# Optimization experiments

Hardware: AMD Instinct MI355X
Metric: run time of the kernel (lower is better)

Reference implementation:

```python
import jax, jax.numpy as jnp
import numpy as np

E = 8   # num_experts
K = 2   # experts per token


def setup_inputs() -> dict:
    key = jax.random.key(0)
    k1, k2, k3, k4 = jax.random.split(key, 4)
    B, S, H, F = 8, 2048, 1024, 2048
    x = jax.random.normal(k1, (B, S, H), jnp.float32)
    Wg = jax.random.normal(k2, (H, E), jnp.float32) * 0.02
    W1 = jax.random.normal(k3, (E, H, F), jnp.float32) * 0.02
    W2 = jax.random.normal(k4, (E, F, H), jnp.float32) * 0.02
    return {"x": x, "Wg": Wg, "W1": W1, "W2": W2}


def reference(x, Wg, W1, W2):
    orig_shape = x.shape
    xt = x.reshape(-1, orig_shape[-1])          # [T, H]
    T = xt.shape[0]

    # router (no jitter noise: training=False path)
    router_logits = xt @ Wg                     # [T, E]
    routing_weights = jax.nn.softmax(router_logits, axis=-1)
    expert_weights, expert_indices = jax.lax.top_k(routing_weights, K)  # [T, K]

    # router z-loss (float32, as in source)
    log_z = jax.nn.logsumexp(router_logits.astype(jnp.float32), axis=-1)
    z_loss = jnp.sum(log_z * log_z) / T

    # load-balancing loss, faithful to source: num_experts taken from
    # router_probs.shape[-1] == K, and one_hot(expert_indices, K)
    # (out-of-range indices -> zero rows under jax.nn.one_hot semantics)
    oh_k = jax.nn.one_hot(expert_indices, K, dtype=jnp.float32)  # [T, K, K]
    expert_mask = jnp.max(oh_k, axis=-2)                          # [T, K]
    tokens_per_expert = jnp.mean(expert_mask, axis=0)             # [K]
    router_prob_per_expert = jnp.mean(expert_weights.astype(jnp.float32), axis=0)  # [K]
    aux_loss = jnp.mean(tokens_per_expert * router_prob_per_expert) * (K ** 2)

    # combine weight per (token, expert): sum of top-k weights routed to e
    cw = jnp.einsum('tk,tke->te', expert_weights,
                    jax.nn.one_hot(expert_indices, E, dtype=expert_weights.dtype))  # [T, E]

    # per-expert MLP, weighted combine (loop over small fixed E)
    out = jnp.zeros_like(xt)
    for e in range(E):
        h = jax.nn.gelu(xt @ W1[e], approximate=False)  # [T, F]
        out = out + cw[:, e:e + 1] * (h @ W2[e])        # [T, H]

    return out.reshape(orig_shape), z_loss, aux_loss
```

## Files before the change

### kernel.cpp

```cpp
#include <hip/hip_runtime.h>
#include <math.h>

#define T_TOKENS 16384
#define H_DIM 1024
#define F_DIM 2048
#define E_NUM 8
#define TPR 72
#define TOT_T (2 * TPR)
#define MAX_PAIRS (TOT_T * 256)

typedef __attribute__((ext_vector_type(8))) short bf16x8;
typedef __attribute__((ext_vector_type(4))) float f32x4;
typedef __attribute__((ext_vector_type(4))) unsigned short us4;

struct TopK { int e0, e1; float w0, w1; };

__device__ __forceinline__ unsigned short f2bf(float f) {
  unsigned int u = __float_as_uint(f);
  u = (u + 0x7fffu + ((u >> 16) & 1u)) >> 16;
  return (unsigned short)u;
}

__device__ __forceinline__ float bf2f(unsigned short u) {
  return __uint_as_float(((unsigned int)u) << 16);
}

__device__ __forceinline__ void gload_lds16(const void* g, void* l) {
  __builtin_amdgcn_global_load_lds(
      (const __attribute__((address_space(1))) void*)g,
      (__attribute__((address_space(3))) void*)l, 16, 0, 0);
}

__device__ __forceinline__ void transpose_body(
    const float* __restrict__ in, unsigned short* __restrict__ out,
    int R, int C, int bx, int by, int e, float* tile ) {
  int r0 = by * 64, c0 = bx * 64;
  int tid = threadIdx.x;
  const float* src = in + ((size_t)e * R + r0) * C + c0;
#pragma unroll
  for (int p = 0; p < 4; p++) {
    int id = p * 256 + tid;
    int row = id >> 4, c4 = (id & 15) * 4;
    float4 v = *(const float4*)&src[(size_t)row * C + c4];
    tile[row * 65 + c4 + 0] = v.x; tile[row * 65 + c4 + 1] = v.y;
    tile[row * 65 + c4 + 2] = v.z; tile[row * 65 + c4 + 3] = v.w;
  }
  __syncthreads();
  unsigned short* dst = out + ((size_t)e * C + c0) * R + r0;
#pragma unroll
  for (int p = 0; p < 4; p++) {
    int id = p * 256 + tid;
    int c = id >> 4, r4 = (id & 15) * 4;
    us4 pk;
#pragma unroll
    for (int j = 0; j < 4; j++) pk[j] = f2bf(tile[(r4 + j) * 65 + c]);
    *(us4*)&dst[(size_t)c * R + r4] = pk;
  }
}

__global__ __launch_bounds__(256) void prep_kernel(
    const float* __restrict__ x, const float* __restrict__ Wg,
    const float* __restrict__ W1, const float* __restrict__ W2,
    unsigned short* __restrict__ xb, unsigned short* __restrict__ w1t,
    unsigned short* __restrict__ w2t, TopK* __restrict__ topk,
    int* __restrict__ counts, float* __restrict__ scal) {
  __shared__ __align__(16) char shraw[E_NUM * H_DIM * 4 + 256];
  int bid = blockIdx.x;
  int tid = threadIdx.x;
  if (bid >= 1024) {
    float* tile = (float*)shraw;
    if (bid < 5120) {
      int lb = bid - 1024;
      transpose_body(W1, w1t, H_DIM, F_DIM, lb & 31, (lb >> 5) & 15, lb >> 9, tile);
    } else {
      int lb = bid - 5120;
      transpose_body(W2, w2t, F_DIM, H_DIM, lb & 15, (lb >> 4) & 31, lb >> 9, tile);
    }
    return;
  }
  float (*wg)[H_DIM] = (float(*)[H_DIM])shraw;
  int* cnt = (int*)(shraw + E_NUM * H_DIM * 4);
  float (*sred)[5] = (float(*)[5])(shraw + E_NUM * H_DIM * 4 + 64);
  if (tid < 16) cnt[tid] = 0;
  for (int i = tid; i < E_NUM * H_DIM; i += 256) wg[i & 7][i >> 3] = Wg[i];
  __syncthreads();
  int lane = tid & 63, wid = tid >> 6;
  float zacc = 0.f, c0 = 0.f, c1 = 0.f, s0 = 0.f, s1 = 0.f;
  int wgid = bid * 4 + wid;
#pragma unroll
  for (int it = 0; it < 4; ++it) {
    int t = wgid + it * 4096;
    const float4* xr = (const float4*)(x + (size_t)t * H_DIM);
    us4* xbr = (us4*)(xb + (size_t)t * H_DIM);
    float l[E_NUM];
#pragma unroll
    for (int e = 0; e < E_NUM; e++) l[e] = 0.f;
#pragma unroll
    for (int i = 0; i < 4; i++) {
      int j = i * 64 + lane;
      float4 v = xr[j];
      us4 pk;
      pk[0] = f2bf(v.x); pk[1] = f2bf(v.y); pk[2] = f2bf(v.z); pk[3] = f2bf(v.w);
      xbr[j] = pk;
      int h = j * 4;
#pragma unroll
      for (int e = 0; e < E_NUM; e++) {
        const f32x4 wv = *(const f32x4*)&wg[e][h];
        l[e] = fmaf(v.x, wv[0], l[e]);
        l[e] = fmaf(v.y, wv[1], l[e]);
        l[e] = fmaf(v.z, wv[2], l[e]);
        l[e] = fmaf(v.w, wv[3], l[e]);
      }
    }
#pragma unroll
    for (int off = 32; off > 0; off >>= 1) {
#pragma unroll
      for (int e = 0; e < E_NUM; e++) l[e] += __shfl_xor(l[e], off, 64);
    }
    if (lane == 0) {
      float mx = l[0];
#pragma unroll
      for (int e = 1; e < E_NUM; e++) mx = fmaxf(mx, l[e]);
      float p[E_NUM]; float se = 0.f;
#pragma unroll
      for (int e = 0; e < E_NUM; e++) { p[e] = expf(l[e] - mx); se += p[e]; }
      float logz = logf(se) + mx;
      int e0 = 0; float b0 = p[0];
#pragma unroll
      for (int e = 1; e < E_NUM; e++) if (p[e] > b0) { b0 = p[e]; e0 = e; }
      int e1 = -1; float b1 = -1.f;
#pragma unroll
      for (int e = 0; e < E_NUM; e++) if (e != e0 && p[e] > b1) { b1 = p[e]; e1 = e; }
      float w0 = b0 / se, w1 = b1 / se;
      TopK tk; tk.e0 = e0; tk.e1 = e1; tk.w0 = w0; tk.w1 = w1;
      topk[t] = tk;
      atomicAdd(&cnt[e0], 1);
      atomicAdd(&cnt[8 + e1], 1);
      zacc += logz * logz;
      c0 += (e0 == 0 || e1 == 0) ? 1.f : 0.f;
      c1 += (e0 == 1 || e1 == 1) ? 1.f : 0.f;
      s0 += w0; s1 += w1;
    }
  }
  if (lane == 0) {
    sred[wid][0] = zacc; sred[wid][1] = c0; sred[wid][2] = c1;
    sred[wid][3] = s0;   sred[wid][4] = s1;
  }
  __syncthreads();
  if (tid == 0) {
    float a[5] = {0.f, 0.f, 0.f, 0.f, 0.f};
    for (int w2 = 0; w2 < 4; w2++)
      for (int k = 0; k < 5; k++) a[k] += sred[w2][k];
    for (int k = 0; k < 5; k++) atomicAdd(&scal[k], a[k]);
  }
  if (tid < 16 && cnt[tid]) atomicAdd(&counts[tid], cnt[tid]);
}

__global__ __launch_bounds__(256) void scan_kernel(
    const int* __restrict__ counts, int* __restrict__ po,
    int* __restrict__ tile_expert) {
  __shared__ int nt[16], start[16];
  int tid = threadIdx.x;
  if (tid < 16) {
    int r = tid >> 3, e = tid & 7;
    int s = 0;
    for (int j = 0; j < e; j++) s += (counts[(r << 3) + j] + 255) >> 8;
    nt[tid] = (counts[tid] + 255) >> 8;
    start[tid] = s;
    po[tid] = r * TPR * 256 + (s << 8);
  }
  __syncthreads();
  for (int ti = tid; ti < TOT_T; ti += 256) {
    int r = ti / TPR, local = ti % TPR;
    int ex = -1;
#pragma unroll
    for (int e = 0; e < E_NUM; e++) {
      int k = (r << 3) + e;
      if (local >= start[k] && local < start[k] + nt[k]) ex = e;
    }
    tile_expert[ti] = ex;
  }
}

__global__ __launch_bounds__(256) void assign_kernel(
    const TopK* __restrict__ topk, const int* __restrict__ po,
    int* __restrict__ cursors, int* __restrict__ pair_token,
    float* __restrict__ pair_w, int* __restrict__ inv0, int* __restrict__ inv1) {
  __shared__ int lcnt[16], lbase[16];
  int tid = threadIdx.x;
  if (tid < 16) lcnt[tid] = 0;
  __syncthreads();
  int t = blockIdx.x * 256 + tid;
  TopK tk = topk[t];
  int li0 = atomicAdd(&lcnt[tk.e0], 1);
  int li1 = atomicAdd(&lcnt[8 + tk.e1], 1);
  __syncthreads();
  if (tid < 16) lbase[tid] = lcnt[tid] ? atomicAdd(&cursors[tid], lcnt[tid]) : 0;
  __syncthreads();
  int p0 = po[tk.e0] + lbase[tk.e0] + li0;
  pair_token[p0] = t; pair_w[p0] = tk.w0; inv0[t] = p0;
  int p1 = po[8 + tk.e1] + lbase[8 + tk.e1] + li1;
  pair_token[p1] = t; pair_w[p1] = tk.w1; inv1[t] = p1;
}

template <int MODE, int K, int N, int NTILES>
__global__ __launch_bounds__(512) void moe_gemm8(
    const unsigned short* __restrict__ A, const unsigned short* __restrict__ Bt,
    const int* __restrict__ pair_token, const float* __restrict__ pair_w,
    const int* __restrict__ tile_expert, int tile_base,
    unsigned short* __restrict__ outbf) {
  constexpr int NBN = N / 256;
  constexpr int NTk = K / 64;
  constexpr int MTC = NTILES / 8;
  constexpr int OSTRIDE = (MODE == 0) ? N : K;
  int l = blockIdx.x;
  int xcd = l & 7, idx = l >> 3;
  int mt = tile_base + xcd * MTC + idx / NBN;
  int nb = idx % NBN;
  int e = tile_expert[mt];
  if (e < 0) return;
  int m0 = mt << 8, n0 = nb << 8;

  extern __shared__ __align__(16) char smem_raw[];
  unsigned short* lds = (unsigned short*)smem_raw;

  int tid = threadIdx.x, lane = tid & 63, wid = tid >> 6;
  int wm = wid >> 2, wn = wid & 3;
  int lo = lane & 15, hi = lane >> 4;
  int l7 = lane & 7;

  int aRB = (wm * 64 + lo) * 64;
  int bRB = (wn * 32 + lo) * 64;
  int kd0 = (hi ^ l7) * 8;
  int kd1 = ((4 + hi) ^ l7) * 8;

  int kcs = ((tid & 7) ^ ((tid >> 3) & 7)) * 8;
  int rr = tid >> 3;
  const unsigned short *aSrc[2][2], *bSrc[2][2];
#pragma unroll
  for (int qa = 0; qa < 2; qa++)
#pragma unroll
    for (int j = 0; j < 2; j++) {
      int row = j * 128 + qa * 64 + rr;
      size_t off;
      if (MODE == 0) {
        int tk = pair_token[m0 + row]; if (tk < 0) tk = 0;
        off = (size_t)tk * K;
      } else {
        off = (size_t)(m0 + row) * K;
      }
      aSrc[qa][j] = A + off + kcs;
    }
#pragma unroll
  for (int qb = 0; qb < 2; qb++)
#pragma unroll
    for (int j = 0; j < 2; j++) {
      int rp = j * 64 + rr;
      int col = (rp >> 5) * 64 + qb * 32 + (rp & 31);
      bSrc[qb][j] = Bt + ((size_t)e * N + n0 + col) * K + kcs;
    }

#define ST0(src, qa, s, sb) do { \
    gload_lds16(src[qa][0] + (size_t)(s) * 64, lds + (sb) + wid * 512); \
    gload_lds16(src[qa][1] + (size_t)(s) * 64, lds + (sb) + 4096 + wid * 512); } while (0)
#define ST_P(ptr, base, g) do { if (g) { \
    gload_lds16(ptr[0], lds + (base) + wid * 512); \
    gload_lds16(ptr[1], lds + (base) + 4096 + wid * 512); \
    ptr[0] += 64; ptr[1] += 64; } } while (0)
#define RD_A(dst, qa, rb) do { _Pragma("unroll") \
    for (int mf = 0; mf < 4; mf++) { \
      dst[mf * 2 + 0] = *(const bf16x8*)&lds[(rb) + (qa) * 8192 + aRB + mf * 1024 + kd0]; \
      dst[mf * 2 + 1] = *(const bf16x8*)&lds[(rb) + (qa) * 8192 + aRB + mf * 1024 + kd1]; } } while (0)
#define RD_B(dst, qb, rb) do { _Pragma("unroll") \
    for (int nf = 0; nf < 2; nf++) { \
      dst[nf * 2 + 0] = *(const bf16x8*)&lds[(rb) + 16384 + (qb) * 8192 + bRB + nf * 1024 + kd0]; \
      dst[nf * 2 + 1] = *(const bf16x8*)&lds[(rb) + 16384 + (qb) * 8192 + bRB + nf * 1024 + kd1]; } } while (0)
#define MMQ(aq, bq, QA, QB) do { __builtin_amdgcn_s_setprio(1); _Pragma("unroll") \
    for (int mf = 0; mf < 4; mf++) _Pragma("unroll") \
    for (int nf = 0; nf < 2; nf++) { \
      acc[(QA) * 4 + mf][(QB) * 2 + nf] = __builtin_amdgcn_mfma_f32_16x16x32_bf16( \
          bq[nf * 2 + 0], aq[mf * 2 + 0], acc[(QA) * 4 + mf][(QB) * 2 + nf], 0, 0, 0); \
      acc[(QA) * 4 + mf][(QB) * 2 + nf] = __builtin_amdgcn_mfma_f32_16x16x32_bf16( \
          bq[nf * 2 + 1], aq[mf * 2 + 1], acc[(QA) * 4 + mf][(QB) * 2 + nf], 0, 0, 0); } \
    __builtin_amdgcn_s_setprio(0); } while (0)
#define PH_BAR() do { asm volatile("s_barrier" ::: "memory"); \
    __builtin_amdgcn_sched_barrier(0); } while (0)
#define VMC(n) do { asm volatile("s_waitcnt vmcnt(" #n ")" ::: "memory"); \
    __builtin_amdgcn_sched_barrier(0); } while (0)

  f32x4 acc[8][4];
#pragma unroll
  for (int i = 0; i < 8; i++)
#pragma unroll
    for (int j = 0; j < 4; j++) acc[i][j] = (f32x4){0.f, 0.f, 0.f, 0.f};

  bf16x8 afr[8], bfr0[4], bfr1[4];

  ST0(aSrc, 0, 0, 0); ST0(bSrc, 0, 0, 16384); ST0(bSrc, 1, 0, 24576); ST0(aSrc, 1, 0, 8192);
  ST0(aSrc, 0, 1, 32768); ST0(bSrc, 0, 1, 32768 + 16384);
  VMC(4); PH_BAR();

  const unsigned short* pB1[2] = {bSrc[1][0] + 64, bSrc[1][1] + 64};
  const unsigned short* pA1[2] = {aSrc[1][0] + 64, aSrc[1][1] + 64};
  const unsigned short* pA0[2] = {aSrc[0][0] + 128, aSrc[0][1] + 128};
  const unsigned short* pB0[2] = {bSrc[0][0] + 128, bSrc[0][1] + 128};

#pragma unroll 2
  for (int t = 0; t < NTk; ++t) {
    int bo = (t & 1) << 15, bn = bo ^ 32768;
    bool g1 = (t + 1 < NTk), g2 = (t + 2 < NTk);
    RD_A(afr, 0, bo);
    RD_B(bfr0, 0, bo);
    ST_P(pB1, bn + 24576, g1);
    VMC(8); PH_BAR();
    MMQ(afr, bfr0, 0, 0);
    RD_B(bfr1, 1, bo);
    ST_P(pA1, bn + 8192, g1);
    PH_BAR();
    MMQ(afr, bfr1, 0, 1);
    RD_A(afr, 1, bo);
    ST_P(pA0, bo, g2);
    VMC(8); PH_BAR();
    MMQ(afr, bfr1, 1, 1);
    ST_P(pB0, bo + 16384, g2);
    PH_BAR();
    MMQ(afr, bfr0, 1, 0);
  }
  asm volatile("s_waitcnt vmcnt(0)" ::: "memory");
  __builtin_amdgcn_sched_barrier(0);
#undef ST0
#undef ST_P
#undef RD_A
#undef RD_B
#undef MMQ
#undef PH_BAR
#undef VMC

#pragma unroll
  for (int mh = 0; mh < 2; mh++)
#pragma unroll
    for (int mf = 0; mf < 4; mf++) {
      size_t p = m0 + wm * 128 + mh * 64 + mf * 16 + lo;
      float w = (MODE == 0) ? 0.f : pair_w[p];
#pragma unroll
      for (int nf = 0; nf < 4; nf++) {
        int f = n0 + wn * 64 + nf * 16 + hi * 4;
        us4 pk;
#pragma unroll
        for (int r = 0; r < 4; r++) {
          float v = acc[mh * 4 + mf][nf][r];
          if (MODE == 0) {
            float u = fmaf(0.044715f * v * v, v, v);
            float s = 1.f / (1.f + __expf(-1.5957691216057308f * u));
            pk[r] = f2bf(v * s);
          } else {
            pk[r] = f2bf(w * v);
          }
        }
        *(us4*)&outbf[p * (size_t)OSTRIDE + f] = pk;
      }
    }
}

__global__ __launch_bounds__(256) void combine_kernel(
    const unsigned short* __restrict__ hout, const int* __restrict__ inv0,
    const int* __restrict__ inv1, float* __restrict__ outp,
    const float* __restrict__ scal) {
  int idx = blockIdx.x * 256 + threadIdx.x;
  int t = idx >> 7;
  int c = (idx & 127) * 8;
  int p0 = inv0[t], p1 = inv1[t];
  bf16x8 va = *(const bf16x8*)&hout[(size_t)p0 * F_DIM + c];
  bf16x8 vb = *(const bf16x8*)&hout[(size_t)p1 * F_DIM + c];
  float* orow = outp + (size_t)t * H_DIM + c;
  float4 o0, o1;
  o0.x = bf2f((unsigned short)va[0]) + bf2f((unsigned short)vb[0]);
  o0.y = bf2f((unsigned short)va[1]) + bf2f((unsigned short)vb[1]);
  o0.z = bf2f((unsigned short)va[2]) + bf2f((unsigned short)vb[2]);
  o0.w = bf2f((unsigned short)va[3]) + bf2f((unsigned short)vb[3]);
  o1.x = bf2f((unsigned short)va[4]) + bf2f((unsigned short)vb[4]);
  o1.y = bf2f((unsigned short)va[5]) + bf2f((unsigned short)vb[5]);
  o1.z = bf2f((unsigned short)va[6]) + bf2f((unsigned short)vb[6]);
  o1.w = bf2f((unsigned short)va[7]) + bf2f((unsigned short)vb[7]);
  *(float4*)&orow[0] = o0;
  *(float4*)&orow[4] = o1;
  if (idx == 0) {
    float invT = 1.f / (float)T_TOKENS;
    float* outTail = outp + (size_t)T_TOKENS * H_DIM;
    outTail[0] = scal[0] * invT;
    float tpe0 = scal[1] * invT, tpe1 = scal[2] * invT;
    float rp0 = scal[3] * invT, rp1 = scal[4] * invT;
    outTail[1] = (tpe0 * rp0 + tpe1 * rp1) * 0.5f * 4.f;
  }
}

extern "C" void kernel_launch(void* const* d_in, const int* in_sizes, int n_in,
                              void* d_out, int out_size, void* d_ws, size_t ws_size,
                              hipStream_t stream) {
  const float* x  = (const float*)d_in[0];
  const float* Wg = (const float*)d_in[1];
  const float* W1 = (const float*)d_in[2];
  const float* W2 = (const float*)d_in[3];
  float* outp = (float*)d_out;

  char* w = (char*)d_ws;
  auto alloc = [&](size_t b) { char* p = w; w += (b + 511) & ~(size_t)511; return p; };
  char*  meta        = alloc(256);
  float* scal        = (float*)(meta + 0);
  int*   counts      = (int*)(meta + 64);
  int*   cursors     = (int*)(meta + 128);
  int*   po          = (int*)alloc(64);
  int*   tile_expert = (int*)alloc(TOT_T * 4);
  TopK*  topk        = (TopK*)alloc((size_t)T_TOKENS * sizeof(TopK));
  int*   pair_token  = (int*)alloc((size_t)MAX_PAIRS * 4);
  float* pair_w      = (float*)alloc((size_t)MAX_PAIRS * 4);
  int*   inv0        = (int*)alloc((size_t)T_TOKENS * 4);
  int*   inv1        = (int*)alloc((size_t)T_TOKENS * 4);
  unsigned short* xb   = (unsigned short*)alloc((size_t)T_TOKENS * H_DIM * 2 + 512);
  unsigned short* w1t  = (unsigned short*)alloc((size_t)E_NUM * F_DIM * H_DIM * 2 + 512);
  unsigned short* hmid = (unsigned short*)alloc((size_t)MAX_PAIRS * F_DIM * 2 + 512);
  unsigned short* w2t = (unsigned short*)d_out;

  hipFuncSetAttribute((const void*)&moe_gemm8<0, H_DIM, F_DIM, TOT_T>,
                      hipFuncAttributeMaxDynamicSharedMemorySize, 131072);
  hipFuncSetAttribute((const void*)&moe_gemm8<1, F_DIM, H_DIM, TOT_T>,
                      hipFuncAttributeMaxDynamicSharedMemorySize, 131072);

  hipMemsetAsync(meta, 0, 256, stream);
  hipMemsetAsync(pair_token, 0xFF, (size_t)MAX_PAIRS * 4, stream);

  dim3 b256(256), b512(512);
  prep_kernel<<<dim3(9216), b256, 0, stream>>>(x, Wg, W1, W2, xb, w1t, w2t,
                                               topk, counts, scal);
  scan_kernel<<<1, b256, 0, stream>>>(counts, po, tile_expert);
  assign_kernel<<<T_TOKENS / 256, b256, 0, stream>>>(topk, po, cursors, pair_token, pair_w,
                                                     inv0, inv1);
  moe_gemm8<0, H_DIM, F_DIM, TOT_T><<<dim3((F_DIM / 256) * TOT_T), b512, 131072, stream>>>(
      xb, w1t, pair_token, pair_w, tile_expert, 0, hmid);
  moe_gemm8<1, F_DIM, H_DIM, TOT_T><<<dim3((H_DIM / 256) * TOT_T), b512, 131072, stream>>>(
      hmid, w2t, pair_token, pair_w, tile_expert, 0, hmid);
  combine_kernel<<<dim3(T_TOKENS * 128 / 256), b256, 0, stream>>>(hmid, inv0, inv1, outp, scal);
}
```

Before: 472.1 us.

## Convert MoE GEMMs to persistent kernels with per-XCD atomic job tickets

Both expert GEMM kernels now launch a fixed grid of 256 persistent blocks instead of one block per (tile, column-block). Each block repeatedly takes a job index from a per-XCD atomic counter and skips empty expert tiles. The goal is to remove launch and exit cost for the many blocks that hit unused padded tiles, and to balance load within each XCD. In exchange it adds atomics and extra barriers per job, and the inner k-loop is no longer unrolled by 2 and now bounds-checks each prefetch.

```diff
diff --git a/kernel.cpp b/kernel.cpp
--- a/kernel.cpp
+++ b/kernel.cpp
@@ -207,22 +207,18 @@
 __global__ __launch_bounds__(512) void moe_gemm8(
     const unsigned short* __restrict__ A, const unsigned short* __restrict__ Bt,
     const int* __restrict__ pair_token, const float* __restrict__ pair_w,
-    const int* __restrict__ tile_expert, int tile_base,
+    const int* __restrict__ tile_expert, int* __restrict__ tickets,
     unsigned short* __restrict__ outbf) {
   constexpr int NBN = N / 256;
   constexpr int NTk = K / 64;
   constexpr int MTC = NTILES / 8;
+  constexpr int JOBS = NBN * MTC;
   constexpr int OSTRIDE = (MODE == 0) ? N : K;
-  int l = blockIdx.x;
-  int xcd = l & 7, idx = l >> 3;
-  int mt = tile_base + xcd * MTC + idx / NBN;
-  int nb = idx % NBN;
-  int e = tile_expert[mt];
-  if (e < 0) return;
-  int m0 = mt << 8, n0 = nb << 8;
+  int xcd = blockIdx.x & 7;
 
   extern __shared__ __align__(16) char smem_raw[];
   unsigned short* lds = (unsigned short*)smem_raw;
+  volatile int* ticket_slot = (volatile int*)lds;
 
   int tid = threadIdx.x, lane = tid & 63, wid = tid >> 6;
   int wm = wid >> 2, wn = wid & 3;
@@ -233,40 +229,15 @@
   int bRB = (wn * 32 + lo) * 64;
   int kd0 = (hi ^ l7) * 8;
   int kd1 = ((4 + hi) ^ l7) * 8;
-
   int kcs = ((tid & 7) ^ ((tid >> 3) & 7)) * 8;
   int rr = tid >> 3;
-  const unsigned short *aSrc[2][2], *bSrc[2][2];
-#pragma unroll
-  for (int qa = 0; qa < 2; qa++)
-#pragma unroll
-    for (int j = 0; j < 2; j++) {
-      int row = j * 128 + qa * 64 + rr;
-      size_t off;
-      if (MODE == 0) {
-        int tk = pair_token[m0 + row]; if (tk < 0) tk = 0;
-        off = (size_t)tk * K;
-      } else {
-        off = (size_t)(m0 + row) * K;
-      }
-      aSrc[qa][j] = A + off + kcs;
-    }
-#pragma unroll
-  for (int qb = 0; qb < 2; qb++)
-#pragma unroll
-    for (int j = 0; j < 2; j++) {
-      int rp = j * 64 + rr;
-      int col = (rp >> 5) * 64 + qb * 32 + (rp & 31);
-      bSrc[qb][j] = Bt + ((size_t)e * N + n0 + col) * K + kcs;
-    }
-
-#define ST0(src, qa, s, sb) do { \
-    gload_lds16(src[qa][0] + (size_t)(s) * 64, lds + (sb) + wid * 512); \
-    gload_lds16(src[qa][1] + (size_t)(s) * 64, lds + (sb) + 4096 + wid * 512); } while (0)
-#define ST_P(ptr, base, g) do { if (g) { \
-    gload_lds16(ptr[0], lds + (base) + wid * 512); \
-    gload_lds16(ptr[1], lds + (base) + 4096 + wid * 512); \
-    ptr[0] += 64; ptr[1] += 64; } } while (0)
+
+#define ST_A(qa, s, sb) do { if ((s) < NTk) { \
+    gload_lds16(aSrc[qa][0] + (size_t)(s) * 64, lds + (sb) + (qa) * 8192 + wid * 512); \
+    gload_lds16(aSrc[qa][1] + (size_t)(s) * 64, lds + (sb) + (qa) * 8192 + 4096 + wid * 512); } } while (0)
+#define ST_B(qb, s, sb) do { if ((s) < NTk) { \
+    gload_lds16(bSrc[qb][0] + (size_t)(s) * 64, lds + (sb) + 16384 + (qb) * 8192 + wid * 512); \
+    gload_lds16(bSrc[qb][1] + (size_t)(s) * 64, lds + (sb) + 16384 + (qb) * 8192 + 4096 + wid * 512); } } while (0)
 #define RD_A(dst, qa, rb) do { _Pragma("unroll") \
     for (int mf = 0; mf < 4; mf++) { \
       dst[mf * 2 + 0] = *(const bf16x8*)&lds[(rb) + (qa) * 8192 + aRB + mf * 1024 + kd0]; \
@@ -288,78 +259,108 @@
 #define VMC(n) do { asm volatile("s_waitcnt vmcnt(" #n ")" ::: "memory"); \
     __builtin_amdgcn_sched_barrier(0); } while (0)
 
-  f32x4 acc[8][4];
-#pragma unroll
-  for (int i = 0; i < 8; i++)
-#pragma unroll
-    for (int j = 0; j < 4; j++) acc[i][j] = (f32x4){0.f, 0.f, 0.f, 0.f};
-
-  bf16x8 afr[8], bfr0[4], bfr1[4];
-
-  ST0(aSrc, 0, 0, 0); ST0(bSrc, 0, 0, 16384); ST0(bSrc, 1, 0, 24576); ST0(aSrc, 1, 0, 8192);
-  ST0(aSrc, 0, 1, 32768); ST0(bSrc, 0, 1, 32768 + 16384);
-  VMC(4); PH_BAR();
-
-  const unsigned short* pB1[2] = {bSrc[1][0] + 64, bSrc[1][1] + 64};
-  const unsigned short* pA1[2] = {aSrc[1][0] + 64, aSrc[1][1] + 64};
-  const unsigned short* pA0[2] = {aSrc[0][0] + 128, aSrc[0][1] + 128};
-  const unsigned short* pB0[2] = {bSrc[0][0] + 128, bSrc[0][1] + 128};
-
-#pragma unroll 2
-  for (int t = 0; t < NTk; ++t) {
-    int bo = (t & 1) << 15, bn = bo ^ 32768;
-    bool g1 = (t + 1 < NTk), g2 = (t + 2 < NTk);
-    RD_A(afr, 0, bo);
-    RD_B(bfr0, 0, bo);
-    ST_P(pB1, bn + 24576, g1);
-    VMC(8); PH_BAR();
-    MMQ(afr, bfr0, 0, 0);
-    RD_B(bfr1, 1, bo);
-    ST_P(pA1, bn + 8192, g1);
-    PH_BAR();
-    MMQ(afr, bfr1, 0, 1);
-    RD_A(afr, 1, bo);
-    ST_P(pA0, bo, g2);
-    VMC(8); PH_BAR();
-    MMQ(afr, bfr1, 1, 1);
-    ST_P(pB0, bo + 16384, g2);
-    PH_BAR();
-    MMQ(afr, bfr0, 1, 0);
-  }
-  asm volatile("s_waitcnt vmcnt(0)" ::: "memory");
-  __builtin_amdgcn_sched_barrier(0);
-#undef ST0
-#undef ST_P
+  for (;;) {
+    if (tid == 0) *ticket_slot = atomicAdd(&tickets[xcd], 1);
+    __syncthreads();
+    int job = *ticket_slot;
+    __syncthreads();
+    if (job >= JOBS) break;
+    int mt = xcd * MTC + job / NBN;
+    int nb = job % NBN;
+    int e = tile_expert[mt];
+    if (e < 0) continue;
+    int m0 = mt << 8, n0 = nb << 8;
+
+    const unsigned short *aSrc[2][2], *bSrc[2][2];
+#pragma unroll
+    for (int qa = 0; qa < 2; qa++)
+#pragma unroll
+      for (int j = 0; j < 2; j++) {
+        int row = j * 128 + qa * 64 + rr;
+        size_t off;
+        if (MODE == 0) {
+          int tk = pair_token[m0 + row]; if (tk < 0) tk = 0;
+          off = (size_t)tk * K;
+        } else {
+          off = (size_t)(m0 + row) * K;
+        }
+        aSrc[qa][j] = A + off + kcs;
+      }
+#pragma unroll
+    for (int qb = 0; qb < 2; qb++)
+#pragma unroll
+      for (int j = 0; j < 2; j++) {
+        int rp = j * 64 + rr;
+        int col = (rp >> 5) * 64 + qb * 32 + (rp & 31);
+        bSrc[qb][j] = Bt + ((size_t)e * N + n0 + col) * K + kcs;
+      }
+
+    f32x4 acc[8][4];
+#pragma unroll
+    for (int i = 0; i < 8; i++)
+#pragma unroll
+      for (int j = 0; j < 4; j++) acc[i][j] = (f32x4){0.f, 0.f, 0.f, 0.f};
+
+    bf16x8 afr[8], bfr0[4], bfr1[4];
+
+    ST_A(0, 0, 0); ST_B(0, 0, 0); ST_B(1, 0, 0); ST_A(1, 0, 0);
+    ST_A(0, 1, 32768); ST_B(0, 1, 32768);
+    VMC(4); PH_BAR();
+
+    for (int t = 0; t < NTk; ++t) {
+      int bo = (t & 1) << 15, bn = bo ^ 32768;
+      RD_A(afr, 0, bo);
+      RD_B(bfr0, 0, bo);
+      ST_B(1, t + 1, bn);
+      VMC(8); PH_BAR();
+      MMQ(afr, bfr0, 0, 0);
+      RD_B(bfr1, 1, bo);
+      ST_A(1, t + 1, bn);
+      PH_BAR();
+      MMQ(afr, bfr1, 0, 1);
+      RD_A(afr, 1, bo);
+      ST_A(0, t + 2, bo);
+      VMC(8); PH_BAR();
+      MMQ(afr, bfr1, 1, 1);
+      ST_B(0, t + 2, bo);
+      PH_BAR();
+      MMQ(afr, bfr0, 1, 0);
+    }
+    asm volatile("s_waitcnt vmcnt(0)" ::: "memory");
+    __builtin_amdgcn_sched_barrier(0);
+
+#pragma unroll
+    for (int mh = 0; mh < 2; mh++)
+#pragma unroll
+      for (int mf = 0; mf < 4; mf++) {
+        size_t p = m0 + wm * 128 + mh * 64 + mf * 16 + lo;
+        float w = (MODE == 0) ? 0.f : pair_w[p];
+#pragma unroll
+        for (int nf = 0; nf < 4; nf++) {
+          int f = n0 + wn * 64 + nf * 16 + hi * 4;
+          us4 pk;
+#pragma unroll
+          for (int r = 0; r < 4; r++) {
+            float v = acc[mh * 4 + mf][nf][r];
+            if (MODE == 0) {
+              float u = fmaf(0.044715f * v * v, v, v);
+              float s = 1.f / (1.f + __expf(-1.5957691216057308f * u));
+              pk[r] = f2bf(v * s);
+            } else {
+              pk[r] = f2bf(w * v);
+            }
+          }
+          *(us4*)&outbf[p * (size_t)OSTRIDE + f] = pk;
+        }
+      }
+  }
+#undef ST_A
+#undef ST_B
 #undef RD_A
 #undef RD_B
 #undef MMQ
 #undef PH_BAR
 #undef VMC
-
-#pragma unroll
-  for (int mh = 0; mh < 2; mh++)
-#pragma unroll
-    for (int mf = 0; mf < 4; mf++) {
-      size_t p = m0 + wm * 128 + mh * 64 + mf * 16 + lo;
-      float w = (MODE == 0) ? 0.f : pair_w[p];
-#pragma unroll
-      for (int nf = 0; nf < 4; nf++) {
-        int f = n0 + wn * 64 + nf * 16 + hi * 4;
-        us4 pk;
-#pragma unroll
-        for (int r = 0; r < 4; r++) {
-          float v = acc[mh * 4 + mf][nf][r];
-          if (MODE == 0) {
-            float u = fmaf(0.044715f * v * v, v, v);
-            float s = 1.f / (1.f + __expf(-1.5957691216057308f * u));
-            pk[r] = f2bf(v * s);
-          } else {
-            pk[r] = f2bf(w * v);
-          }
-        }
-        *(us4*)&outbf[p * (size_t)OSTRIDE + f] = pk;
-      }
-    }
 }
 
 __global__ __launch_bounds__(256) void combine_kernel(
@@ -409,6 +410,8 @@
   float* scal        = (float*)(meta + 0);
   int*   counts      = (int*)(meta + 64);
   int*   cursors     = (int*)(meta + 128);
+  int*   tickets1    = (int*)(meta + 192);
+  int*   tickets2    = (int*)(meta + 224);
   int*   po          = (int*)alloc(64);
   int*   tile_expert = (int*)alloc(TOT_T * 4);
   TopK*  topk        = (TopK*)alloc((size_t)T_TOKENS * sizeof(TopK));
@@ -435,9 +438,9 @@
   scan_kernel<<<1, b256, 0, stream>>>(counts, po, tile_expert);
   assign_kernel<<<T_TOKENS / 256, b256, 0, stream>>>(topk, po, cursors, pair_token, pair_w,
                                                      inv0, inv1);
-  moe_gemm8<0, H_DIM, F_DIM, TOT_T><<<dim3((F_DIM / 256) * TOT_T), b512, 131072, stream>>>(
-      xb, w1t, pair_token, pair_w, tile_expert, 0, hmid);
-  moe_gemm8<1, F_DIM, H_DIM, TOT_T><<<dim3((H_DIM / 256) * TOT_T), b512, 131072, stream>>>(
-      hmid, w2t, pair_token, pair_w, tile_expert, 0, hmid);
+  moe_gemm8<0, H_DIM, F_DIM, TOT_T><<<dim3(256), b512, 131072, stream>>>(
+      xb, w1t, pair_token, pair_w, tile_expert, tickets1, hmid);
+  moe_gemm8<1, F_DIM, H_DIM, TOT_T><<<dim3(256), b512, 131072, stream>>>(
+      hmid, w2t, pair_token, pair_w, tile_expert, tickets2, hmid);
   combine_kernel<<<dim3(T_TOKENS * 128 / 256), b256, 0, stream>>>(hmid, inv0, inv1, outp, scal);
 }
```

Result: slower. 538.7 us (+14.1%).
